# Kernel optimization log

Measured on AMD Instinct MI355X. Metric: run time of the kernel, lower is better.

Reference implementation:

```python
import jax, jax.numpy as jnp
import numpy as np

EPS = 1e-7


def setup_inputs() -> dict:
    key = jax.random.key(0)
    k1, k2, k3 = jax.random.split(key, 3)
    B, IN, OUT = 256, 256, 512
    x = jax.random.uniform(k1, (B, IN), dtype=jnp.float32)
    w = jax.random.uniform(k2, (IN, OUT), dtype=jnp.float32)
    t = jax.random.uniform(k3, (B, OUT), dtype=jnp.float32)
    return {"x": x, "w": w, "t": t}


def reference(x, w, t):
    # x: [B, IN], w: [IN, OUT], t: [B, OUT]
    xe = x[:, :, None]          # [B, IN, 1]
    te = t[:, None, :]          # [B, 1, OUT]
    we = w[None, :, :]          # [1, IN, OUT]

    one = jnp.asarray(1.0, dtype=x.dtype)
    # rel_x: relevance of x, reduced over batch dim 0 -> [1, IN, OUT]
    rel_x = jnp.minimum(te / (xe + EPS), one).sum(axis=0, keepdims=True) \
            / xe.sum(axis=0, keepdims=True)
    # rel_w: relevance of w, reduced over IN dim -> [B, 1, OUT]
    rel_w = jnp.minimum(te / (we + EPS), one).sum(axis=-2, keepdims=True) \
            / xe.sum(axis=-2, keepdims=True)

    ind_x = jnp.argmax(xe * rel_x, axis=-2, keepdims=True)  # [B, 1, OUT]
    ind_w = jnp.argmax(rel_w * we, axis=-2, keepdims=True)  # [B, 1, OUT]

    inner_x = xe * jax.lax.stop_gradient(we)  # [B, IN, OUT]
    inner_w = jax.lax.stop_gradient(xe) * we  # [B, IN, OUT]

    chosen_x = jnp.take_along_axis(inner_x, ind_x, axis=-2).squeeze(-2)  # [B, OUT]
    chosen_w = jnp.take_along_axis(inner_w, ind_w, axis=-2).squeeze(-2)  # [B, OUT]
    return chosen_x, chosen_w
```

## Files before the change

kernel.cpp:

```cpp
#include <hip/hip_runtime.h>

constexpr int B   = 256;
constexpr int IN  = 256;
constexpr int OUT = 512;
constexpr double EPSD = 1e-7;


__global__ __launch_bounds__(256) void k_setup(const float* __restrict__ x,
        double* __restrict__ rxd, double* __restrict__ part, float* __restrict__ xt) {
    const int tid = threadIdx.x;
    const int blk = blockIdx.x;
    if (blk < 32) {
        const int b0 = blk * 8;
        #pragma unroll
        for (int k = 0; k < 8; ++k)
            rxd[(b0 + k) * IN + tid] = 1.0 / ((double)x[(b0 + k) * IN + tid] + EPSD);
    } else if (blk < 40) {
        const int j = blk - 32, b0 = j * 32;
        double s0 = 0, s1 = 0, s2 = 0, s3 = 0;
        #pragma unroll
        for (int k = 0; k < 32; k += 4) {
            s0 += (double)x[(b0 + k + 0) * IN + tid];
            s1 += (double)x[(b0 + k + 1) * IN + tid];
            s2 += (double)x[(b0 + k + 2) * IN + tid];
            s3 += (double)x[(b0 + k + 3) * IN + tid];
        }
        part[j * IN + tid] = (s0 + s1) + (s2 + s3);
    } else {
        const int i0 = (blk - 40) * 32;
        for (int k = 0; k < 32; ++k)
            xt[(i0 + k) * B + tid] = x[tid * IN + (i0 + k)];
    }
}

__global__ __launch_bounds__(512, 2) void k_main(const float* __restrict__ w,
        const float* __restrict__ t, const double* __restrict__ rxd,
        const double* __restrict__ part, const float* __restrict__ xt,
        float* __restrict__ out) {
    const int tid  = threadIdx.x;
    const int half = tid >> 8;
    const int j    = tid & 255;
    const int o    = blockIdx.x * 2 + half;

    __shared__ double tc[2 * B];
    __shared__ double rc[2 * IN];
    __shared__ unsigned long long swv[8];

    {
        float wv = w[j * OUT + o];
        unsigned long long key =
            ((unsigned long long)__float_as_uint(wv) << 8) | (unsigned)(255 - j);
        #pragma unroll
        for (int off = 32; off; off >>= 1) {
            unsigned long long v = __shfl_down(key, off);
            key = v > key ? v : key;
        }
        if ((tid & 63) == 0) swv[tid >> 6] = key;
    }

    tc[half * B + j] = (double)t[j * OUT + o];
    double ps = 0.0;
    #pragma unroll
    for (int k = 0; k < 8; ++k) ps += part[k * IN + j];
    const double rcolv = 1.0 / ps;
    __syncthreads();

    unsigned long long wk = swv[half * 4];
    #pragma unroll
    for (int k = 1; k < 4; ++k) {
        unsigned long long v = swv[half * 4 + k];
        wk = v > wk ? v : wk;
    }
    const int warg_o = 255 - (int)(wk & 0xFFull);

    {
        const double* __restrict__ rx  = rxd + j;
        const double* __restrict__ tcc = tc + half * B;
        double a0 = 0, a1 = 0, a2 = 0, a3 = 0;
        #pragma unroll 2
        for (int b = 0; b < B; b += 4) {
            a0 += fmin(tcc[b + 0] * rx[(b + 0) * IN], 1.0);
            a1 += fmin(tcc[b + 1] * rx[(b + 1) * IN], 1.0);
            a2 += fmin(tcc[b + 2] * rx[(b + 2) * IN], 1.0);
            a3 += fmin(tcc[b + 3] * rx[(b + 3) * IN], 1.0);
        }
        rc[half * IN + j] = ((a0 + a1) + (a2 + a3)) * rcolv;
    }
    __syncthreads();

    const int b = j;
    const double* __restrict__ rcc = rc + half * IN;
    double m0 = -1.0, m1 = -1.0, m2 = -1.0, m3 = -1.0;
    #pragma unroll 2
    for (int i = 0; i < IN; i += 4) {
        double s0 = (double)xt[(i + 0) * B + b] * rcc[i + 0];
        double s1 = (double)xt[(i + 1) * B + b] * rcc[i + 1];
        double s2 = (double)xt[(i + 2) * B + b] * rcc[i + 2];
        double s3 = (double)xt[(i + 3) * B + b] * rcc[i + 3];
        long long u0 = (__double_as_longlong(s0) & ~0xFFll) | (long long)(255 - (i + 0));
        long long u1 = (__double_as_longlong(s1) & ~0xFFll) | (long long)(255 - (i + 1));
        long long u2 = (__double_as_longlong(s2) & ~0xFFll) | (long long)(255 - (i + 2));
        long long u3 = (__double_as_longlong(s3) & ~0xFFll) | (long long)(255 - (i + 3));
        m0 = fmax(m0, __longlong_as_double(u0));
        m1 = fmax(m1, __longlong_as_double(u1));
        m2 = fmax(m2, __longlong_as_double(u2));
        m3 = fmax(m3, __longlong_as_double(u3));
    }
    double m = fmax(fmax(m0, m1), fmax(m2, m3));
    const int ia = 255 - (int)(__double_as_longlong(m) & 0xFF);

    float* __restrict__ out0 = out;
    float* __restrict__ out1 = out + (size_t)B * OUT;
    out0[b * OUT + o] = xt[ia * B + b] * w[ia * OUT + o];

    const int iw = (tc[half * B + b] > 0.0) ? warg_o : 0;
    out1[b * OUT + o] = xt[iw * B + b] * w[iw * OUT + o];
}

extern "C" void kernel_launch(void* const* d_in, const int* in_sizes, int n_in,
                              void* d_out, int out_size, void* d_ws, size_t ws_size,
                              hipStream_t stream) {
    const float* x = (const float*)d_in[0];
    const float* w = (const float*)d_in[1];
    const float* t = (const float*)d_in[2];
    float* out = (float*)d_out;

    double* dws  = (double*)d_ws;
    double* RXD  = dws;
    double* PART = RXD + (size_t)B * IN;
    float*  XT   = (float*)(PART + 8 * IN);

    k_setup<<<48, 256, 0, stream>>>(x, RXD, PART, XT);
    k_main<<<OUT / 2, 512, 0, stream>>>(w, t, RXD, PART, XT, out);
}
```

Baseline: 91.56 us.

## Split reductions across thread halves with vectorized double2/float2 loads

```diff
diff --git a/kernel.cpp b/kernel.cpp
--- a/kernel.cpp
+++ b/kernel.cpp
@@ -4,6 +4,8 @@
 constexpr int IN  = 256;
 constexpr int OUT = 512;
 constexpr double EPSD = 1e-7;
+
+typedef unsigned long long ull;
 
 
 __global__ __launch_bounds__(256) void k_setup(const float* __restrict__ x,
@@ -42,79 +44,98 @@
     const int j    = tid & 255;
     const int o    = blockIdx.x * 2 + half;
 
-    __shared__ double tc[2 * B];
-    __shared__ double rc[2 * IN];
-    __shared__ unsigned long long swv[8];
+    __shared__ double tc[2][B];
+    __shared__ double rp[2][2][IN];
+    __shared__ double rc[2][IN];
+    __shared__ ull    keys[2][2][B];
+    __shared__ ull    swv[8];
 
     {
         float wv = w[j * OUT + o];
-        unsigned long long key =
-            ((unsigned long long)__float_as_uint(wv) << 8) | (unsigned)(255 - j);
+        ull key = ((ull)__float_as_uint(wv) << 8) | (unsigned)(255 - j);
         #pragma unroll
         for (int off = 32; off; off >>= 1) {
-            unsigned long long v = __shfl_down(key, off);
+            ull v = __shfl_down(key, off);
             key = v > key ? v : key;
         }
         if ((tid & 63) == 0) swv[tid >> 6] = key;
     }
 
-    tc[half * B + j] = (double)t[j * OUT + o];
+    tc[half][j] = (double)t[j * OUT + o];
     double ps = 0.0;
     #pragma unroll
     for (int k = 0; k < 8; ++k) ps += part[k * IN + j];
     const double rcolv = 1.0 / ps;
     __syncthreads();
 
-    unsigned long long wk = swv[half * 4];
+    ull wk = swv[half * 4];
     #pragma unroll
-    for (int k = 1; k < 4; ++k) {
-        unsigned long long v = swv[half * 4 + k];
-        wk = v > wk ? v : wk;
-    }
+    for (int k = 1; k < 4; ++k) { ull v = swv[half * 4 + k]; wk = v > wk ? v : wk; }
     const int warg_o = 255 - (int)(wk & 0xFFull);
 
     {
-        const double* __restrict__ rx  = rxd + j;
-        const double* __restrict__ tcc = tc + half * B;
+        const int i0 = (j & 127) * 2;
+        const int bh = j >> 7;
+        const double* __restrict__ tcc  = tc[half] + bh * 128;
+        const double* __restrict__ base = rxd + (size_t)(bh * 128) * IN + i0;
         double a0 = 0, a1 = 0, a2 = 0, a3 = 0;
-        #pragma unroll 2
-        for (int b = 0; b < B; b += 4) {
-            a0 += fmin(tcc[b + 0] * rx[(b + 0) * IN], 1.0);
-            a1 += fmin(tcc[b + 1] * rx[(b + 1) * IN], 1.0);
-            a2 += fmin(tcc[b + 2] * rx[(b + 2) * IN], 1.0);
-            a3 += fmin(tcc[b + 3] * rx[(b + 3) * IN], 1.0);
+        #pragma unroll 8
+        for (int k = 0; k < 128; k += 2) {
+            double2 r0 = *(const double2*)(base + (size_t)k * IN);
+            double2 r1 = *(const double2*)(base + (size_t)(k + 1) * IN);
+            double t0 = tcc[k], t1 = tcc[k + 1];
+            a0 += fmin(t0 * r0.x, 1.0);
+            a1 += fmin(t0 * r0.y, 1.0);
+            a2 += fmin(t1 * r1.x, 1.0);
+            a3 += fmin(t1 * r1.y, 1.0);
         }
-        rc[half * IN + j] = ((a0 + a1) + (a2 + a3)) * rcolv;
+        rp[half][bh][i0]     = a0 + a2;
+        rp[half][bh][i0 + 1] = a1 + a3;
+    }
+    __syncthreads();
+    rc[half][j] = (rp[half][0][j] + rp[half][1][j]) * rcolv;
+    __syncthreads();
+
+    {
+        const int b0 = (j & 127) * 2;
+        const int ih = j >> 7;
+        const double* __restrict__ rcc = rc[half];
+        double mA0 = -1.0, mA1 = -1.0, mB0 = -1.0, mB1 = -1.0;
+        #pragma unroll 8
+        for (int i = ih * 128; i < ih * 128 + 128; i += 2) {
+            float2 x0 = *(const float2*)&xt[(size_t)i * B + b0];
+            float2 x1 = *(const float2*)&xt[(size_t)(i + 1) * B + b0];
+            double s00 = (double)x0.x * rcc[i];
+            double s01 = (double)x0.y * rcc[i];
+            double s10 = (double)x1.x * rcc[i + 1];
+            double s11 = (double)x1.y * rcc[i + 1];
+            long long u00 = (__double_as_longlong(s00) & ~0xFFll) | (long long)(255 - i);
+            long long u01 = (__double_as_longlong(s01) & ~0xFFll) | (long long)(255 - i);
+            long long u10 = (__double_as_longlong(s10) & ~0xFFll) | (long long)(255 - (i + 1));
+            long long u11 = (__double_as_longlong(s11) & ~0xFFll) | (long long)(255 - (i + 1));
+            mA0 = fmax(mA0, __longlong_as_double(u00));
+            mB0 = fmax(mB0, __longlong_as_double(u01));
+            mA1 = fmax(mA1, __longlong_as_double(u10));
+            mB1 = fmax(mB1, __longlong_as_double(u11));
+        }
+        keys[half][ih][b0]     = (ull)__double_as_longlong(fmax(mA0, mA1));
+        keys[half][ih][b0 + 1] = (ull)__double_as_longlong(fmax(mB0, mB1));
     }
     __syncthreads();
 
-    const int b = j;
-    const double* __restrict__ rcc = rc + half * IN;
-    double m0 = -1.0, m1 = -1.0, m2 = -1.0, m3 = -1.0;
-    #pragma unroll 2
-    for (int i = 0; i < IN; i += 4) {
-        double s0 = (double)xt[(i + 0) * B + b] * rcc[i + 0];
-        double s1 = (double)xt[(i + 1) * B + b] * rcc[i + 1];
-        double s2 = (double)xt[(i + 2) * B + b] * rcc[i + 2];
-        double s3 = (double)xt[(i + 3) * B + b] * rcc[i + 3];
-        long long u0 = (__double_as_longlong(s0) & ~0xFFll) | (long long)(255 - (i + 0));
-        long long u1 = (__double_as_longlong(s1) & ~0xFFll) | (long long)(255 - (i + 1));
-        long long u2 = (__double_as_longlong(s2) & ~0xFFll) | (long long)(255 - (i + 2));
-        long long u3 = (__double_as_longlong(s3) & ~0xFFll) | (long long)(255 - (i + 3));
-        m0 = fmax(m0, __longlong_as_double(u0));
-        m1 = fmax(m1, __longlong_as_double(u1));
-        m2 = fmax(m2, __longlong_as_double(u2));
-        m3 = fmax(m3, __longlong_as_double(u3));
+    {
+        const int b = (j & 127) * 2 + (j >> 7);
+        ull k0 = keys[half][0][b], k1 = keys[half][1][b];
+        ull mk = k0 > k1 ? k0 : k1;
+        const int ia = 255 - (int)(mk & 0xFFull);
+
+        float* __restrict__ out0 = out;
+        float* __restrict__ out1 = out + (size_t)B * OUT;
+        out0[b * OUT + o] = xt[(size_t)ia * B + b] * w[ia * OUT + o];
+
+        const int iw = (tc[half][b] > 0.0) ? warg_o : 0;
+        out1[b * OUT + o] = xt[(size_t)iw * B + b] * w[iw * OUT + o];
     }
-    double m = fmax(fmax(m0, m1), fmax(m2, m3));
-    const int ia = 255 - (int)(__double_as_longlong(m) & 0xFF);
-
-    float* __restrict__ out0 = out;
-    float* __restrict__ out1 = out + (size_t)B * OUT;
-    out0[b * OUT + o] = xt[ia * B + b] * w[ia * OUT + o];
-
-    const int iw = (tc[half * B + b] > 0.0) ? warg_o : 0;
-    out1[b * OUT + o] = xt[iw * B + b] * w[iw * OUT + o];
 }
 
 extern "C" void kernel_launch(void* const* d_in, const int* in_sizes, int n_in,
```

New measurement: 83.64 us. 1.09x faster.
